# Optimization experiments

Measured on AMD Instinct MI355X. Metric: run time of the kernel, lower is better.

The kernel has to match this reference:

```python
import jax, jax.numpy as jnp
import numpy as np

NUM_RBF = 16
RBF_D_MIN, RBF_D_MAX = 2.0, 22.0
CB_A, CB_B, CB_C = -0.58273431, 0.56802827, -0.54067466
TOP_K = 32
MAX_REL = 32
NPOS = 16
HID = 128
LN_EPS = 1e-5


def _gather_nodes(nodes, idx):
    # nodes: (B, L, D), idx: (B, L, K) -> (B, L, K, D)
    return jax.vmap(lambda n, i: n[i])(nodes, idx)


def _rbf_encode(D):
    mu = jnp.linspace(RBF_D_MIN, RBF_D_MAX, NUM_RBF, dtype=D.dtype)
    sigma = (RBF_D_MAX - RBF_D_MIN) / NUM_RBF
    return jnp.exp(-((D[..., None] - mu) ** 2) / (sigma ** 2))


def setup_inputs() -> dict:
    key = jax.random.key(0)
    ks = jax.random.split(key, 4)
    B, L = 2, 2048
    X = jax.random.normal(ks[0], (B, L, 4, 3), jnp.float32) * 10.0
    residue_mask = jnp.ones((B, L), jnp.float32)
    R_idx = jnp.arange(B * L, dtype=jnp.int32).reshape(B, L)
    chain_labels = jnp.zeros((B, L), jnp.int32)
    # learned params
    W_pos = jax.random.normal(ks[1], (NPOS, 2 * MAX_REL + 2), jnp.float32) * 0.05
    b_pos = jnp.zeros((NPOS,), jnp.float32)
    W_edge = jax.random.normal(ks[2], (HID, 25 * NUM_RBF + NPOS), jnp.float32) * 0.02
    ln_gamma = jnp.ones((HID,), jnp.float32)
    ln_beta = jnp.zeros((HID,), jnp.float32)
    return {"X": X, "residue_mask": residue_mask, "R_idx": R_idx,
            "chain_labels": chain_labels, "W_pos": W_pos, "b_pos": b_pos,
            "W_edge": W_edge, "ln_gamma": ln_gamma, "ln_beta": ln_beta}


def reference(X, residue_mask, R_idx, chain_labels, W_pos, b_pos, W_edge, ln_gamma, ln_beta):
    B, L = X.shape[0], X.shape[1]
    K = min(TOP_K, L)
    # virtual CB from backbone N, CA, C
    N, CA, C = X[..., 0, :], X[..., 1, :], X[..., 2, :]
    b = CA - N
    c = C - CA
    a = jnp.cross(b, c, axis=-1)
    CB = (CB_A * a + CB_B * b + CB_C * c + CA)[..., None, :]
    atoms_5 = jnp.concatenate([X, CB], axis=-2)  # (B, L, 5, 3)
    # kNN on CA coords with invalid residues pushed far away
    diff = CA[:, :, None, :] - CA[:, None, :, :]
    dist_sq = jnp.sum(diff * diff, axis=-1)  # (B, L, L)
    inv_mask = 1.0 - residue_mask
    dist_sq = dist_sq + inv_mask[:, None, :] * 1e6
    _, E_idx = jax.lax.top_k(-dist_sq, K)  # smallest-k indices, (B, L, K)
    # gather neighbor 5-atom coords and compute 25 pairwise distances
    Xf = atoms_5.reshape(B, L, 15)
    Xg = _gather_nodes(Xf, E_idx).reshape(B, L, K, 5, 3)
    d2 = jnp.sum((atoms_5[:, :, None, :, None, :] - Xg[:, :, :, None, :, :]) ** 2, axis=-1)
    D = jnp.sqrt(d2 + 1e-6)  # (B, L, K, 5, 5)
    rbf = _rbf_encode(D).reshape(B, L, K, 25 * NUM_RBF)
    # positional encodings (standard ProteinMPNN form)
    Rg = _gather_nodes(R_idx[..., None], E_idx)[..., 0]  # (B, L, K)
    Cg = _gather_nodes(chain_labels[..., None], E_idx)[..., 0]
    d_rel = Rg - R_idx[:, :, None]
    same_chain = (Cg == chain_labels[:, :, None])
    d_clip = jnp.clip(d_rel + MAX_REL, 0, 2 * MAX_REL)
    d_final = jnp.where(same_chain, d_clip, 2 * MAX_REL + 1)
    oh = jax.nn.one_hot(d_final, 2 * MAX_REL + 2, dtype=rbf.dtype)
    pos_enc = jnp.einsum('blkc,pc->blkp', oh, W_pos) + b_pos
    # edge embedding + layernorm
    edge_input = jnp.concatenate([pos_enc, rbf], axis=-1)  # (B, L, K, 416)
    h = jnp.einsum('blkf,hf->blkh', edge_input, W_edge)
    mean = jnp.mean(h, axis=-1, keepdims=True)
    var = jnp.var(h, axis=-1, keepdims=True)
    E = (h - mean) * jax.lax.rsqrt(var + LN_EPS) * ln_gamma + ln_beta
    return E_idx, E
```

## Files before the change

kernel.cpp:

```cpp
#include <hip/hip_runtime.h>
#include <hip/hip_bf16.h>

#define LEN   2048
#define KNB   32
#define HID   128
#define FS    440
#define FBSZ  (32 * FS)
#define NST   19

typedef unsigned long long ull;
typedef unsigned int uint32;
typedef float f32x4  __attribute__((ext_vector_type(4)));
typedef float f32x16 __attribute__((ext_vector_type(16)));

__device__ __forceinline__ void bar_lgkm() {
    asm volatile("s_waitcnt lgkmcnt(0)" ::: "memory");
    __builtin_amdgcn_s_barrier();
    asm volatile("" ::: "memory");
}

__global__ __launch_bounds__(256) void topk_kernel(
    const float* __restrict__ X, const float* __restrict__ mask,
    const float* __restrict__ W_edge, int* __restrict__ Wf8,
    float* __restrict__ eidx_out) {
    const int bid = blockIdx.x;
    const int tid = threadIdx.x;

    if (bid >= 2 * LEN) {
        const int t = (bid - 2 * LEN) * 256 + tid;
        if (t < 13312) {
            const float4 w = ((const float4*)W_edge)[t];
            int r = __builtin_amdgcn_cvt_pk_fp8_f32(w.x, w.y, 0, false);
            r = __builtin_amdgcn_cvt_pk_fp8_f32(w.z, w.w, r, true);
            Wf8[t] = r;
        }
        return;
    }

    const int row = bid;
    const int b = row >> 11;
    const int i = row & (LEN - 1);

    __shared__ int hist[512];
    __shared__ ull cand[LEN];
    __shared__ int candcnt;
    __shared__ int selB;

    const float* Xb = X + (size_t)b * LEN * 12;
    const float* mb = mask + (size_t)b * LEN;
    const float cax = Xb[i * 12 + 3];
    const float cay = Xb[i * 12 + 4];
    const float caz = Xb[i * 12 + 5];

    uint32 d2b[8];
#pragma unroll
    for (int q = 0; q < 8; ++q) {
        const int j = q * 256 + tid;
        const float4 ld0 = *(const float4*)(Xb + j * 12);
        const float4 ld1 = *(const float4*)(Xb + j * 12 + 4);
        float dx = __fsub_rn(cax, ld0.w);
        float dy = __fsub_rn(cay, ld1.x);
        float dz = __fsub_rn(caz, ld1.y);
        float d2 = __fadd_rn(__fadd_rn(__fmul_rn(dx, dx), __fmul_rn(dy, dy)),
                             __fmul_rn(dz, dz));
        d2 = __fadd_rn(d2, __fmul_rn(__fsub_rn(1.0f, mb[j]), 1000000.0f));
        d2b[q] = __float_as_uint(d2);
    }

    hist[tid] = 0; hist[tid + 256] = 0;
    if (tid == 0) candcnt = 0;
    __syncthreads();
#pragma unroll
    for (int q = 0; q < 8; ++q) atomicAdd(&hist[d2b[q] >> 22], 1);
    __syncthreads();

    if (tid < 64) {
        int loc[8];
        int s = 0;
#pragma unroll
        for (int t = 0; t < 8; ++t) { loc[t] = hist[tid * 8 + t]; s += loc[t]; }
        int incl = s;
#pragma unroll
        for (int off = 1; off < 64; off <<= 1) {
            int o = __shfl_up(incl, off, 64);
            if (tid >= off) incl += o;
        }
        const int excl = incl - s;
        if (excl < KNB && incl >= KNB) {
            int c = excl;
#pragma unroll
            for (int t = 0; t < 8; ++t) {
                int c2 = c + loc[t];
                if (c < KNB && c2 >= KNB) selB = tid * 8 + t;
                c = c2;
            }
        }
    }
    __syncthreads();
    const uint32 B = (uint32)selB;

#pragma unroll
    for (int q = 0; q < 8; ++q) {
        if ((d2b[q] >> 22) <= B) {
            int p = atomicAdd(&candcnt, 1);
            cand[p] = (((ull)d2b[q]) << 32) | (uint32)(q * 256 + tid);
        }
    }
    __syncthreads();
    const int M = candcnt;

    for (int c = tid; c < M; c += 256) {
        const ull k = cand[c];
        int r = 0;
        for (int m = 0; m < M; ++m) r += (cand[m] < k);
        if (r < KNB)
            eidx_out[(size_t)row * KNB + r] = (float)(uint32)(k & 0xFFFFFFFFull);
    }
}

__device__ __forceinline__ void load_res_atoms_bf(const float* __restrict__ p, __bf16* dst) {
    const float Nx = p[0], Ny = p[1], Nz = p[2];
    const float Ax = p[3], Ay = p[4], Az = p[5];
    const float Cx = p[6], Cy = p[7], Cz = p[8];
    const float Ox = p[9], Oy = p[10], Oz = p[11];
    const float bx = Ax - Nx, by = Ay - Ny, bz = Az - Nz;
    const float cx = Cx - Ax, cy = Cy - Ay, cz = Cz - Az;
    const float axv = by * cz - bz * cy;
    const float ayv = bz * cx - bx * cz;
    const float azv = bx * cy - by * cx;
    dst[0] = (__bf16)Nx;  dst[1] = (__bf16)Ny;  dst[2] = (__bf16)Nz;
    dst[3] = (__bf16)Ax;  dst[4] = (__bf16)Ay;  dst[5] = (__bf16)Az;
    dst[6] = (__bf16)Cx;  dst[7] = (__bf16)Cy;  dst[8] = (__bf16)Cz;
    dst[9] = (__bf16)Ox;  dst[10] = (__bf16)Oy; dst[11] = (__bf16)Oz;
    dst[12] = (__bf16)(-0.58273431f * axv + 0.56802827f * bx + -0.54067466f * cx + Ax);
    dst[13] = (__bf16)(-0.58273431f * ayv + 0.56802827f * by + -0.54067466f * cy + Ay);
    dst[14] = (__bf16)(-0.58273431f * azv + 0.56802827f * bz + -0.54067466f * cz + Az);
}

__device__ __forceinline__ int pk4(float a, float b, float c, float d) {
    int r = __builtin_amdgcn_cvt_pk_fp8_f32(a, b, 0, false);
    return __builtin_amdgcn_cvt_pk_fp8_f32(c, d, r, true);
}

#define E1  3.2053337e-1f
#define E3  3.2931300e-2f
#define E5  3.3834001e-3f
#define E7  3.4760500e-4f

__device__ __forceinline__ void compute_features(
    int tid, int Ri, int Ci,
    const __bf16* __restrict__ wposL,
    const int* jR, const int* jC,
    const __bf16 (*natoms)[NST], const __bf16* iatoms,
    unsigned char* featF8) {
#pragma unroll
    for (int it = 0; it < 2; ++it) {
        const int task = tid + it * 256;
        const int e = task >> 4, p = task & 15;
        const int drel = jR[e] - Ri;
        const int same = (jC[e] == Ci);
        int dc = drel + 32;
        dc = dc < 0 ? 0 : (dc > 64 ? 64 : dc);
        const int df = same ? dc : 65;
        const float v = (float)wposL[p * 66 + df];
        const int pb = __builtin_amdgcn_cvt_pk_fp8_f32(v, 0.0f, 0, false);
        featF8[e * FS + p] = (unsigned char)(pb & 0xFF);
    }
    for (int task = tid; task < 800; task += 256) {
        const int mn = task >> 5, e = task & 31;
        const int m = mn / 5, n = mn - m * 5;
        const float ax = (float)iatoms[m * 3 + 0];
        const float ay = (float)iatoms[m * 3 + 1];
        const float az = (float)iatoms[m * 3 + 2];
        const float dx = ax - (float)natoms[e][n * 3 + 0];
        const float dy = ay - (float)natoms[e][n * 3 + 1];
        const float dz = az - (float)natoms[e][n * 3 + 2];
        const float D = sqrtf(dx * dx + dy * dy + dz * dz + 1e-6f);
        const float Dc = fminf(D, 40.0f);
        const float v4 = Dc - 7.3333333f;
        const float A4  = __expf(-0.64f * v4 * v4);
        const float C4  = __expf(1.7066667f * v4);
        const float Ci4 = 1.0f / C4;
        ull lo, hi2;
        {
            const float f3 = A4 * Ci4 * E1;
            const float f2 = f3 * Ci4 * E3;
            const float f1 = f2 * Ci4 * E5;
            const float f0 = f1 * Ci4 * E7;
            const float f5 = A4 * C4 * E1;
            const float f6 = f5 * C4 * E3;
            const float f7 = f6 * C4 * E5;
            lo = (uint32)pk4(f0, f1, f2, f3)
               | ((ull)(uint32)pk4(A4, f5, f6, f7) << 32);
        }
        const float v12 = Dc - 18.0f;
        const float A12  = __expf(-0.64f * v12 * v12);
        const float C12  = C4 * 1.24140e-8f;
        const float Ci12 = Ci4 * 8.05543e7f;
        {
            const float f11 = A12 * Ci12 * E1;
            const float f10 = f11 * Ci12 * E3;
            const float f9  = f10 * Ci12 * E5;
            const float f8  = f9  * Ci12 * E7;
            const float f13 = A12 * C12 * E1;
            const float f14 = f13 * C12 * E3;
            const float f15 = f14 * C12 * E5;
            hi2 = (uint32)pk4(f8, f9, f10, f11)
                | ((ull)(uint32)pk4(A12, f13, f14, f15) << 32);
        }
        *(ull*)(featF8 + e * FS + 16 + mn * 16)     = lo;
        *(ull*)(featF8 + e * FS + 16 + mn * 16 + 8) = hi2;
    }
}

__device__ __forceinline__ f32x16 gemm26(const unsigned char* fb, const long* wreg) {
    f32x16 acc = {0.f, 0.f, 0.f, 0.f, 0.f, 0.f, 0.f, 0.f,
                  0.f, 0.f, 0.f, 0.f, 0.f, 0.f, 0.f, 0.f};
#pragma unroll
    for (int ks = 0; ks < 26; ++ks) {
        const long a = *(const long*)(fb + ks * 16);
        acc = __builtin_amdgcn_mfma_f32_32x32x16_fp8_fp8(wreg[ks], a, acc, 0, 0, 0);
    }
    return acc;
}

__device__ __forceinline__ void partials(
    const f32x16& acc, float (*pSb)[4], float (*pQb)[4],
    int e32, int cg, int hi) {
    float s = 0.f, q = 0.f;
#pragma unroll
    for (int r = 0; r < 16; ++r) { s += acc[r]; q += acc[r] * acc[r]; }
    s += __shfl_xor(s, 32, 64);
    q += __shfl_xor(q, 32, 64);
    if (hi == 0) { pSb[e32][cg] = s; pQb[e32][cg] = q; }
}

__device__ __forceinline__ void ln_store(
    const f32x16& acc, const float (*pSb)[4], const float (*pQb)[4],
    int e32, int cg, int hi, int myrow,
    const float* gbuf, const float* bbuf, float* __restrict__ outE) {
    const float4 ps = *(const float4*)&pSb[e32][0];
    const float4 pq = *(const float4*)&pQb[e32][0];
    const float s = ps.x + ps.y + ps.z + ps.w;
    const float q = pq.x + pq.y + pq.z + pq.w;
    const float mean = s * (1.0f / 128.0f);
    const float rstd = rsqrtf(q * (1.0f / 128.0f) - mean * mean + 1e-5f);
    const int cb = cg * 32 + hi * 4;
    float* orow = outE + ((size_t)myrow * KNB + e32) * HID + cb;
#pragma unroll
    for (int j = 0; j < 4; ++j) {
        const float4 gg = *(const float4*)&gbuf[cb + 8 * j];
        const float4 bb = *(const float4*)&bbuf[cb + 8 * j];
        float4 o;
        o.x = (acc[4 * j + 0] - mean) * rstd * gg.x + bb.x;
        o.y = (acc[4 * j + 1] - mean) * rstd * gg.y + bb.y;
        o.z = (acc[4 * j + 2] - mean) * rstd * gg.z + bb.z;
        o.w = (acc[4 * j + 3] - mean) * rstd * gg.w + bb.w;
        *(float4*)(orow + 8 * j) = o;
    }
}

__global__ __launch_bounds__(256, 4) void edge_kernel(
    const float* __restrict__ X,
    const int* __restrict__ Ridx, const int* __restrict__ Chain,
    const float* __restrict__ W_pos, const float* __restrict__ b_pos,
    const unsigned char* __restrict__ Wf8,
    const float* __restrict__ lng, const float* __restrict__ lnb,
    const float* __restrict__ eidx_f, float* __restrict__ outE) {
    const int tid = threadIdx.x;
    const int row0 = blockIdx.x * 4;
    const int b = row0 >> 11;
    const int i0 = row0 & (LEN - 1);

    __shared__ __align__(16) unsigned char featF8[2][FBSZ];
    __shared__ __align__(4) __bf16 natoms[4][32][NST];
    __shared__ __bf16 iatoms[4][16];
    __shared__ __bf16 wposL[16 * 66];
    __shared__ __align__(16) float pS[2][32][4], pQ[2][32][4];
    __shared__ float gbuf[HID], bbuf[HID];
    __shared__ int jR[4][KNB], jC[4][KNB];
    __shared__ int riS[4], ciS[4];

    const float* Xb = X + (size_t)b * LEN * 12;

    const int cg = tid >> 6, l = tid & 63;
    const int e32 = l & 31, hi = l >> 5;

    long wreg[26];
    {
        const unsigned char* wb = Wf8 + (size_t)(cg * 32 + e32) * 416 + hi * 8;
#pragma unroll
        for (int ks = 0; ks < 26; ++ks)
            wreg[ks] = *(const long*)(wb + ks * 16);
    }

    for (int t = tid; t < 1056; t += 256)
        wposL[t] = (__bf16)(W_pos[t] + b_pos[t / 66]);
    if (tid < 128) {
        const int r = tid >> 5, e = tid & 31;
        const int j = (int)eidx_f[(size_t)(row0 + r) * KNB + e];
        jR[r][e] = Ridx[b * LEN + j];
        jC[r][e] = Chain[b * LEN + j];
        load_res_atoms_bf(Xb + j * 12, &natoms[r][e][0]);
        gbuf[tid] = lng[tid];
        bbuf[tid] = lnb[tid];
    } else if (tid < 132) {
        const int r = tid - 128;
        load_res_atoms_bf(Xb + (size_t)(i0 + r) * 12, &iatoms[r][0]);
    } else if (tid < 136) {
        riS[tid - 132] = Ridx[b * LEN + i0 + (tid - 132)];
    } else if (tid < 140) {
        ciS[tid - 136] = Chain[b * LEN + i0 + (tid - 136)];
    }
    bar_lgkm();

    compute_features(tid, riS[0], ciS[0], wposL, jR[0], jC[0],
                     natoms[0], iatoms[0], featF8[0]);
    bar_lgkm();

    const unsigned char* fb0 = featF8[0] + e32 * FS + hi * 8;
    const unsigned char* fb1 = featF8[1] + e32 * FS + hi * 8;
    f32x16 acc;

    acc = gemm26(fb0, wreg);
    compute_features(tid, riS[1], ciS[1], wposL, jR[1], jC[1],
                     natoms[1], iatoms[1], featF8[1]);
    partials(acc, pS[0], pQ[0], e32, cg, hi);
    bar_lgkm();

    ln_store(acc, pS[0], pQ[0], e32, cg, hi, row0 + 0, gbuf, bbuf, outE);
    acc = gemm26(fb1, wreg);
    compute_features(tid, riS[2], ciS[2], wposL, jR[2], jC[2],
                     natoms[2], iatoms[2], featF8[0]);
    partials(acc, pS[1], pQ[1], e32, cg, hi);
    bar_lgkm();

    ln_store(acc, pS[1], pQ[1], e32, cg, hi, row0 + 1, gbuf, bbuf, outE);
    acc = gemm26(fb0, wreg);
    compute_features(tid, riS[3], ciS[3], wposL, jR[3], jC[3],
                     natoms[3], iatoms[3], featF8[1]);
    partials(acc, pS[0], pQ[0], e32, cg, hi);
    bar_lgkm();

    ln_store(acc, pS[0], pQ[0], e32, cg, hi, row0 + 2, gbuf, bbuf, outE);
    acc = gemm26(fb1, wreg);
    partials(acc, pS[1], pQ[1], e32, cg, hi);
    bar_lgkm();

    ln_store(acc, pS[1], pQ[1], e32, cg, hi, row0 + 3, gbuf, bbuf, outE);
}

extern "C" void kernel_launch(void* const* d_in, const int* in_sizes, int n_in,
                              void* d_out, int out_size, void* d_ws, size_t ws_size,
                              hipStream_t stream) {
    const float* X      = (const float*)d_in[0];
    const float* mask   = (const float*)d_in[1];
    const int*   Ridx   = (const int*)d_in[2];
    const int*   Chain  = (const int*)d_in[3];
    const float* W_pos  = (const float*)d_in[4];
    const float* b_pos  = (const float*)d_in[5];
    const float* W_edge = (const float*)d_in[6];
    const float* lng    = (const float*)d_in[7];
    const float* lnb    = (const float*)d_in[8];

    float* out  = (float*)d_out;
    float* eidx = out;
    float* E    = out + (size_t)2 * LEN * KNB;

    unsigned char* Wf8 = (unsigned char*)d_ws;

    const int nrow = 2 * LEN;
    topk_kernel<<<nrow + 52, 256, 0, stream>>>(X, mask, W_edge, (int*)Wf8, eidx);
    edge_kernel<<<nrow / 4, 256, 0, stream>>>(X, Ridx, Chain, W_pos, b_pos, Wf8,
                                              lng, lnb, eidx, E);
}
```

Baseline: 53.34 us.

## Process four query rows per top-k block with CA coords cached in LDS

The top-k kernel now handles four query rows per block instead of one. It stages all CA coordinates plus the mask penalty for the batch in shared memory once, then reuses them for each row's distance, histogram and selection pass. This cuts the number of blocks and the repeated global loads of the coordinate array, at the cost of 32KB more LDS and less parallelism (1024 blocks instead of 4096). Separately, the MFMA loop in the edge kernel is wrapped in s_setprio raises to favour matrix-issue waves.

Result: slower. 65.94 us (+23.6%).

```diff
diff --git a/kernel.cpp b/kernel.cpp
--- a/kernel.cpp
+++ b/kernel.cpp
@@ -26,8 +26,8 @@
     const int bid = blockIdx.x;
     const int tid = threadIdx.x;
 
-    if (bid >= 2 * LEN) {
-        const int t = (bid - 2 * LEN) * 256 + tid;
+    if (bid >= 1024) {
+        const int t = (bid - 1024) * 256 + tid;
         if (t < 13312) {
             const float4 w = ((const float4*)W_edge)[t];
             int r = __builtin_amdgcn_cvt_pk_fp8_f32(w.x, w.y, 0, false);
@@ -37,10 +37,11 @@
         return;
     }
 
-    const int row = bid;
-    const int b = row >> 11;
-    const int i = row & (LEN - 1);
-
+    const int row0 = bid * 4;
+    const int b = row0 >> 11;
+    const int i0 = row0 & (LEN - 1);
+
+    __shared__ __align__(16) float4 caL[LEN];
     __shared__ int hist[512];
     __shared__ ull cand[LEN];
     __shared__ int candcnt;
@@ -48,73 +49,84 @@
 
     const float* Xb = X + (size_t)b * LEN * 12;
     const float* mb = mask + (size_t)b * LEN;
-    const float cax = Xb[i * 12 + 3];
-    const float cay = Xb[i * 12 + 4];
-    const float caz = Xb[i * 12 + 5];
-
-    uint32 d2b[8];
+
 #pragma unroll
     for (int q = 0; q < 8; ++q) {
         const int j = q * 256 + tid;
         const float4 ld0 = *(const float4*)(Xb + j * 12);
         const float4 ld1 = *(const float4*)(Xb + j * 12 + 4);
-        float dx = __fsub_rn(cax, ld0.w);
-        float dy = __fsub_rn(cay, ld1.x);
-        float dz = __fsub_rn(caz, ld1.y);
-        float d2 = __fadd_rn(__fadd_rn(__fmul_rn(dx, dx), __fmul_rn(dy, dy)),
-                             __fmul_rn(dz, dz));
-        d2 = __fadd_rn(d2, __fmul_rn(__fsub_rn(1.0f, mb[j]), 1000000.0f));
-        d2b[q] = __float_as_uint(d2);
-    }
-
-    hist[tid] = 0; hist[tid + 256] = 0;
-    if (tid == 0) candcnt = 0;
+        caL[j] = make_float4(ld0.w, ld1.x, ld1.y,
+                             __fmul_rn(__fsub_rn(1.0f, mb[j]), 1000000.0f));
+    }
     __syncthreads();
-#pragma unroll
-    for (int q = 0; q < 8; ++q) atomicAdd(&hist[d2b[q] >> 22], 1);
-    __syncthreads();
-
-    if (tid < 64) {
-        int loc[8];
-        int s = 0;
-#pragma unroll
-        for (int t = 0; t < 8; ++t) { loc[t] = hist[tid * 8 + t]; s += loc[t]; }
-        int incl = s;
-#pragma unroll
-        for (int off = 1; off < 64; off <<= 1) {
-            int o = __shfl_up(incl, off, 64);
-            if (tid >= off) incl += o;
-        }
-        const int excl = incl - s;
-        if (excl < KNB && incl >= KNB) {
-            int c = excl;
-#pragma unroll
-            for (int t = 0; t < 8; ++t) {
-                int c2 = c + loc[t];
-                if (c < KNB && c2 >= KNB) selB = tid * 8 + t;
-                c = c2;
+
+    for (int r = 0; r < 4; ++r) {
+        const float4 ci = caL[i0 + r];
+
+        uint32 d2b[8];
+#pragma unroll
+        for (int q = 0; q < 8; ++q) {
+            const float4 cj = caL[q * 256 + tid];
+            float dx = __fsub_rn(ci.x, cj.x);
+            float dy = __fsub_rn(ci.y, cj.y);
+            float dz = __fsub_rn(ci.z, cj.z);
+            float d2 = __fadd_rn(__fadd_rn(__fmul_rn(dx, dx), __fmul_rn(dy, dy)),
+                                 __fmul_rn(dz, dz));
+            d2 = __fadd_rn(d2, cj.w);
+            d2b[q] = __float_as_uint(d2);
+        }
+
+        hist[tid] = 0; hist[tid + 256] = 0;
+        if (tid == 0) candcnt = 0;
+        __syncthreads();
+#pragma unroll
+        for (int q = 0; q < 8; ++q) atomicAdd(&hist[d2b[q] >> 22], 1);
+        __syncthreads();
+
+        if (tid < 64) {
+            int loc[8];
+            int s = 0;
+#pragma unroll
+            for (int t = 0; t < 8; ++t) { loc[t] = hist[tid * 8 + t]; s += loc[t]; }
+            int incl = s;
+#pragma unroll
+            for (int off = 1; off < 64; off <<= 1) {
+                int o = __shfl_up(incl, off, 64);
+                if (tid >= off) incl += o;
             }
-        }
-    }
-    __syncthreads();
-    const uint32 B = (uint32)selB;
-
-#pragma unroll
-    for (int q = 0; q < 8; ++q) {
-        if ((d2b[q] >> 22) <= B) {
-            int p = atomicAdd(&candcnt, 1);
-            cand[p] = (((ull)d2b[q]) << 32) | (uint32)(q * 256 + tid);
-        }
-    }
-    __syncthreads();
-    const int M = candcnt;
-
-    for (int c = tid; c < M; c += 256) {
-        const ull k = cand[c];
-        int r = 0;
-        for (int m = 0; m < M; ++m) r += (cand[m] < k);
-        if (r < KNB)
-            eidx_out[(size_t)row * KNB + r] = (float)(uint32)(k & 0xFFFFFFFFull);
+            const int excl = incl - s;
+            if (excl < KNB && incl >= KNB) {
+                int c = excl;
+#pragma unroll
+                for (int t = 0; t < 8; ++t) {
+                    int c2 = c + loc[t];
+                    if (c < KNB && c2 >= KNB) selB = tid * 8 + t;
+                    c = c2;
+                }
+            }
+        }
+        __syncthreads();
+        const uint32 B = (uint32)selB;
+
+#pragma unroll
+        for (int q = 0; q < 8; ++q) {
+            if ((d2b[q] >> 22) <= B) {
+                int p = atomicAdd(&candcnt, 1);
+                cand[p] = (((ull)d2b[q]) << 32) | (uint32)(q * 256 + tid);
+            }
+        }
+        __syncthreads();
+        const int M = candcnt;
+
+        for (int c = tid; c < M; c += 256) {
+            const ull k = cand[c];
+            int rk = 0;
+            for (int m = 0; m < M; ++m) rk += (cand[m] < k);
+            if (rk < KNB)
+                eidx_out[(size_t)(row0 + r) * KNB + rk] =
+                    (float)(uint32)(k & 0xFFFFFFFFull);
+        }
+        __syncthreads();
     }
 }
 
@@ -216,11 +228,13 @@
 __device__ __forceinline__ f32x16 gemm26(const unsigned char* fb, const long* wreg) {
     f32x16 acc = {0.f, 0.f, 0.f, 0.f, 0.f, 0.f, 0.f, 0.f,
                   0.f, 0.f, 0.f, 0.f, 0.f, 0.f, 0.f, 0.f};
+    __builtin_amdgcn_s_setprio(1);
 #pragma unroll
     for (int ks = 0; ks < 26; ++ks) {
         const long a = *(const long*)(fb + ks * 16);
         acc = __builtin_amdgcn_mfma_f32_32x32x16_fp8_fp8(wreg[ks], a, acc, 0, 0, 0);
     }
+    __builtin_amdgcn_s_setprio(0);
     return acc;
 }
 
@@ -370,7 +384,7 @@
     unsigned char* Wf8 = (unsigned char*)d_ws;
 
     const int nrow = 2 * LEN;
-    topk_kernel<<<nrow + 52, 256, 0, stream>>>(X, mask, W_edge, (int*)Wf8, eidx);
+    topk_kernel<<<nrow / 4 + 52, 256, 0, stream>>>(X, mask, W_edge, (int*)Wf8, eidx);
     edge_kernel<<<nrow / 4, 256, 0, stream>>>(X, Ridx, Chain, W_pos, b_pos, Wf8,
                                               lng, lnb, eidx, E);
 }
```
